# Kernel tuning notes

Measured on AMD Instinct MI355X. Metric: run time of the kernel, lower is better.

Reference implementation:

```python
import jax, jax.numpy as jnp
import numpy as np

B, C, HK, WK = 1, 128, 32, 32
S = 4                       # upsample factor hq/hk = dilation
HQ, WQ = HK * S, WK * S
NH = 4                      # heads
HD = C // NH                # head dim
KH = KW = 7                 # odd(max(3, round(2*0.1*32)))
DH = DW = S
EPS = float(jnp.finfo(jnp.float32).eps)  # torch RMSNorm default eps for fp32


def natten_indices(L, K, D):
    """NATTEN clamped-window key indices per query position. Returns [L, K] int array."""
    NS = K // 2
    i = np.arange(L)
    if D <= 1:
        start = np.maximum(i - NS, 0) + (i + NS >= L) * (L - i - NS - 1)
    else:
        ni = i - NS * D
        imodd = i % D
        a = (L // D) * D
        b = L - a
        far = np.where(imodd < b, L - b + imodd - 2 * NS * D, a + imodd - K * D)
        start = np.where(ni < 0, imodd, np.where(i + NS * D >= L, far, ni))
    return jnp.asarray(start[:, None] + np.arange(K)[None, :] * D)


def setup_inputs() -> dict:
    key = jax.random.key(0)
    ks = jax.random.split(key, 8)
    sc = 1.0 / np.sqrt(C)
    return {
        "q": jax.random.normal(ks[0], (B, C, HQ, WQ), jnp.float32),
        "k": jax.random.normal(ks[1], (B, C, HK, WK), jnp.float32),
        "v": jax.random.normal(ks[2], (B, C, HK, WK), jnp.float32),
        "conv_w": jax.random.normal(ks[3], (C, C, 3, 3), jnp.float32) * (sc / 3.0),
        "normq_w": 1.0 + 0.02 * jax.random.normal(ks[4], (C,), jnp.float32),
        "normk_w": 1.0 + 0.02 * jax.random.normal(ks[5], (C,), jnp.float32),
        "qproj_w": jax.random.normal(ks[6], (C, C), jnp.float32) * sc,
        "qproj_b": jnp.zeros((C,), jnp.float32),
        "kproj_w": jax.random.normal(ks[7], (C, C), jnp.float32) * sc,
        "kproj_b": jnp.zeros((C,), jnp.float32),
    }


def _rmsnorm(x, w):  # x: [B,C,H,W]; RMS over channel dim
    ms = jnp.mean(x * x, axis=1, keepdims=True)
    return x * jax.lax.rsqrt(ms + EPS) * w[None, :, None, None]


def reference(q, k, v, conv_w, normq_w, normk_w, qproj_w, qproj_b, kproj_w, kproj_b):
    # 3x3 conv on q (no bias, padding=1)
    q = jax.lax.conv_general_dilated(q, conv_w, (1, 1), "SAME",
                                     dimension_numbers=("NCHW", "OIHW", "NCHW"))
    q = _rmsnorm(q, normq_w)
    k = _rmsnorm(k, normk_w)
    # 1x1 projections (Conv2d k=1 with bias)
    q = jnp.einsum("oc,bchw->bohw", qproj_w, q) + qproj_b[None, :, None, None]
    k = jnp.einsum("oc,bchw->bohw", kproj_w, k) + kproj_b[None, :, None, None]
    # nearest-exact upsample of k, v to (HQ, WQ); integer factor -> exact pixel repeat
    k = jnp.repeat(jnp.repeat(k, S, axis=2), S, axis=3)
    v = jnp.repeat(jnp.repeat(v, S, axis=2), S, axis=3)
    # NATTEN layout [B, H, W, heads, hd]
    qn = q.reshape(B, NH, HD, HQ, WQ).transpose(0, 3, 4, 1, 2)
    kn = k.reshape(B, NH, HD, HQ, WQ).transpose(0, 3, 4, 1, 2)
    vh = v.transpose(0, 2, 3, 1)  # [B,HQ,WQ,C]; V is shared (expanded) across heads.
    # channel-pad-to-8 in the original is a no-op here since C % 8 == 0.
    ih = natten_indices(HQ, KH, DH)  # [HQ, KH]
    iw = natten_indices(WQ, KW, DW)  # [WQ, KW]
    k_nb = jnp.take(jnp.take(kn, ih, axis=1), iw, axis=3)  # [B,HQ,KH,WQ,KW,NH,HD]
    v_nb = jnp.take(jnp.take(vh, ih, axis=1), iw, axis=3)  # [B,HQ,KH,WQ,KW,C]
    scale = HD ** -0.5
    logits = jnp.einsum("bijhd,bimjnhd->bijhmn", qn, k_nb) * scale
    attn = jax.nn.softmax(logits.reshape(B, HQ, WQ, NH, KH * KW), axis=-1)
    attn = attn.reshape(B, HQ, WQ, NH, KH, KW)
    # heads share V, and the block takes mean over heads at the end; the mean
    # commutes with the (linear) V-contraction, so average attention first.
    attn_mean = attn.mean(axis=3)  # [B,HQ,WQ,KH,KW]
    out = jnp.einsum("bijmn,bimjnc->bcij", attn_mean, v_nb)  # [B,C,HQ,WQ]
    return out
```

## Files before the change

### kernel.cpp

```cpp
#include <hip/hip_runtime.h>

#define EPS_ 1.1920928955078125e-07f
#define SCALE_ 0.17677669529663687f

typedef __attribute__((ext_vector_type(8))) short s8b;
typedef __attribute__((ext_vector_type(4))) float f32x4;

static __device__ __forceinline__ unsigned short f2bf(float f) {
  unsigned int u = __float_as_uint(f);
  unsigned int r = (u + 0x7fffu + ((u >> 16) & 1u)) >> 16;
  return (unsigned short)r;
}
static __device__ __forceinline__ int S_(int c) {
  return (c < 3) ? 0 : ((c > 28) ? 25 : (c - 3));
}

__global__ __launch_bounds__(256) void wpack_k(
    const float* __restrict__ cw, const float* __restrict__ qw,
    const float* __restrict__ nqw, const float* __restrict__ kw,
    const float* __restrict__ nkw, unsigned short* __restrict__ wb,
    unsigned short* __restrict__ wnq, unsigned short* __restrict__ wnk) {
  int idx = blockIdx.x * 256 + threadIdx.x;
  if (idx < 147456) {
    int i32 = idx & 31, r = idx >> 5;
    int oc = r & 127, r2 = r >> 7;
    int kc = r2 & 3, t = r2 >> 2;
    wb[idx] = f2bf(cw[oc * 1152 + (kc * 32 + i32) * 9 + t]);
  } else if (idx < 163840) {
    int j = idx - 147456;
    wnq[j] = f2bf(qw[j] * nqw[j & 127]);
  } else if (idx < 180224) {
    int j = idx - 163840;
    wnk[j] = f2bf(kw[j] * nkw[j & 127]);
  }
}

__global__ __launch_bounds__(512) void fused_k(
    const float* __restrict__ q_in, const float* __restrict__ k_in,
    const float* __restrict__ v_in, const unsigned short* __restrict__ wb,
    const unsigned short* __restrict__ wnq, const unsigned short* __restrict__ wnk,
    const float* __restrict__ qbias, const float* __restrict__ kbias,
    float* __restrict__ out) {
  __shared__ __align__(16) char smem[65344];
  unsigned short* in_l = (unsigned short*)smem;
  unsigned short* qc_l = (unsigned short*)smem;
  unsigned short* a_l  = (unsigned short*)smem;
  float* o_l   = (float*)smem;
  unsigned short* kx_l = (unsigned short*)(smem + 27200);
  unsigned short* v_l  = (unsigned short*)(smem + 44608);
  float* red_l = (float*)(smem + 63040);
  float* rs_l  = (float*)(smem + 65088);

  const int tid = threadIdx.x;
  const int CY = blockIdx.x >> 4, CX = blockIdx.x & 15;
  const int Y0 = CY * 8, X0 = CX * 8;
  const int w = tid >> 6, lane = tid & 63;
  const int lm = lane & 15, kg = lane >> 4;
  const int mg = w & 1, ng = w >> 1;
  const int h = w >> 1, mh = w & 1;

  const int sy0 = S_(2 * CY), sy1 = S_(2 * CY + 1);
  const int sx0 = S_(2 * CX), sx1 = S_(2 * CX + 1);
  const int kyb = min(sy0, 24), kxb = min(sx0, 24);
  const int oy0 = sy0 - kyb, oy1 = sy1 - kyb;
  const int ox0 = sx0 - kxb, ox1 = sx1 - kxb;

  for (int i = tid; i < 12800; i += 512) {
    int c = i / 100, r = i - c * 100;
    int ry = r / 10, rx = r - ry * 10;
    int gy = Y0 - 1 + ry, gx = X0 - 1 + rx;
    float v = 0.f;
    if ((unsigned)gy < 128u && (unsigned)gx < 128u) v = q_in[c * 16384 + gy * 128 + gx];
    in_l[r * 136 + c] = f2bf(v);
  }
  {
    const int j = tid & 63, cg = tid >> 3 >> 3;
    const int ky = j >> 3, kx = j & 7;
    const float* kp = &k_in[(kyb + ky) * 32 + kxb + kx];
    float s = 0.f;
#pragma unroll
    for (int it = 0; it < 16; it++) {
      int c = cg * 16 + it;
      float v = kp[c * 1024];
      s += v * v;
      kx_l[j * 136 + c] = f2bf(v);
    }
    red_l[j * 8 + cg] = s;
  }
  {
    const int j = tid & 63, cg = tid >> 6;
    const int ky = j >> 3, kx = j & 7;
    const float* vp = &v_in[(kyb + ky) * 32 + kxb + kx];
#pragma unroll
    for (int it = 0; it < 16; it++) {
      int c = cg * 16 + it;
      v_l[c * 72 + j] = f2bf(vp[c * 1024]);
    }
  }
  __syncthreads();

  if (tid < 64) {
    float s = 0.f;
#pragma unroll
    for (int e = 0; e < 8; e++) s += red_l[tid * 8 + e];
    rs_l[tid] = rsqrtf(s * (1.f / 128.f) + EPS_);
  }
  __syncthreads();

  {
    f32x4 ka[4];
#pragma unroll
    for (int a = 0; a < 4; a++) ka[a] = (f32x4){0.f, 0.f, 0.f, 0.f};
#pragma unroll
    for (int kc = 0; kc < 4; kc++) {
      s8b af[4];
#pragma unroll
      for (int mt = 0; mt < 4; mt++)
        af[mt] = *(const s8b*)&wnk[((mg * 4 + mt) * 16 + lm) * 128 + kc * 32 + kg * 8];
      s8b bf = *(const s8b*)&kx_l[(ng * 16 + lm) * 136 + kc * 32 + kg * 8];
#pragma unroll
      for (int mt = 0; mt < 4; mt++)
        ka[mt] = __builtin_amdgcn_mfma_f32_16x16x32_bf16(af[mt], bf, ka[mt], 0, 0, 0);
    }
    __syncthreads();
    const int px = ng * 16 + lm;
    const float rs = rs_l[px];
#pragma unroll
    for (int mt = 0; mt < 4; mt++)
#pragma unroll
      for (int r = 0; r < 4; r++) {
        int c = (mg * 4 + mt) * 16 + kg * 4 + r;
        kx_l[px * 136 + c] = f2bf(kbias[c] + rs * ka[mt][r]);
      }
  }

  f32x4 acc[4];
#pragma unroll
  for (int a = 0; a < 4; a++) acc[a] = (f32x4){0.f, 0.f, 0.f, 0.f};
  const int pxc = ng * 16 + lm;
  const int qy = pxc >> 3, qx = pxc & 7;
#pragma unroll
  for (int t = 0; t < 9; t++) {
    const int dy = t / 3, dx = t - (t / 3) * 3;
#pragma unroll
    for (int kc = 0; kc < 4; kc++) {
      const unsigned short* wp = wb + (t * 4 + kc) * 4096;
      s8b af[4];
#pragma unroll
      for (int mt = 0; mt < 4; mt++)
        af[mt] = *(const s8b*)&wp[((mg * 4 + mt) * 16 + lm) * 32 + kg * 8];
      s8b bf = *(const s8b*)&in_l[((qy + dy) * 10 + qx + dx) * 136 + kc * 32 + kg * 8];
#pragma unroll
      for (int mt = 0; mt < 4; mt++)
        acc[mt] = __builtin_amdgcn_mfma_f32_16x16x32_bf16(af[mt], bf, acc[mt], 0, 0, 0);
    }
  }
  __syncthreads();
#pragma unroll
  for (int mt = 0; mt < 4; mt++)
#pragma unroll
    for (int r = 0; r < 4; r++) {
      int c = (mg * 4 + mt) * 16 + kg * 4 + r;
      qc_l[pxc * 136 + c] = f2bf(acc[mt][r]);
    }
  __syncthreads();

  {
    int px = tid >> 3, t8 = tid & 7;
    const unsigned short* row = &qc_l[px * 136 + t8 * 16];
    s8b v0 = *(const s8b*)row;
    s8b v1 = *(const s8b*)(row + 8);
    float s = 0.f;
#pragma unroll
    for (int e = 0; e < 8; e++) {
      float f0 = __uint_as_float(((unsigned)(unsigned short)v0[e]) << 16);
      float f1 = __uint_as_float(((unsigned)(unsigned short)v1[e]) << 16);
      s += f0 * f0 + f1 * f1;
    }
    red_l[px * 8 + t8] = s;
  }
  __syncthreads();
  if (tid < 64) {
    float s = 0.f;
#pragma unroll
    for (int e = 0; e < 8; e++) s += red_l[tid * 8 + e];
    rs_l[tid] = rsqrtf(s * (1.f / 128.f) + EPS_);
  }
  __syncthreads();

  {
    f32x4 qa[4];
#pragma unroll
    for (int a = 0; a < 4; a++) qa[a] = (f32x4){0.f, 0.f, 0.f, 0.f};
#pragma unroll
    for (int kc = 0; kc < 4; kc++) {
      s8b af[4];
#pragma unroll
      for (int mt = 0; mt < 4; mt++)
        af[mt] = *(const s8b*)&wnq[((mg * 4 + mt) * 16 + lm) * 128 + kc * 32 + kg * 8];
      s8b bf = *(const s8b*)&qc_l[(ng * 16 + lm) * 136 + kc * 32 + kg * 8];
#pragma unroll
      for (int mt = 0; mt < 4; mt++)
        qa[mt] = __builtin_amdgcn_mfma_f32_16x16x32_bf16(af[mt], bf, qa[mt], 0, 0, 0);
    }
    __syncthreads();
    const int px = ng * 16 + lm;
    const float rs = rs_l[px];
#pragma unroll
    for (int mt = 0; mt < 4; mt++)
#pragma unroll
      for (int r = 0; r < 4; r++) {
        int c = (mg * 4 + mt) * 16 + kg * 4 + r;
        qc_l[px * 136 + c] = f2bf(qbias[c] + rs * qa[mt][r]);
      }
  }
  __syncthreads();

  f32x4 lg[2][4];
  {
    s8b qa[2], kb[4];
#pragma unroll
    for (int mt = 0; mt < 2; mt++)
      qa[mt] = *(const s8b*)&qc_l[((mh * 2 + mt) * 16 + lm) * 136 + h * 32 + kg * 8];
#pragma unroll
    for (int nt = 0; nt < 4; nt++)
      kb[nt] = *(const s8b*)&kx_l[(nt * 16 + lm) * 136 + h * 32 + kg * 8];
#pragma unroll
    for (int mt = 0; mt < 2; mt++)
#pragma unroll
      for (int nt = 0; nt < 4; nt++)
        lg[mt][nt] = __builtin_amdgcn_mfma_f32_16x16x32_bf16(
            qa[mt], kb[nt], (f32x4){0.f, 0.f, 0.f, 0.f}, 0, 0, 0);
  }
  __syncthreads();

  {
    const int kyA = lm >> 3, kxq = lm & 7;
    const bool kxv0 = (unsigned)(kxq - ox0) < 7u;
    const bool kxv1 = (unsigned)(kxq - ox1) < 7u;
#pragma unroll
    for (int mt = 0; mt < 2; mt++) {
#pragma unroll
      for (int r = 0; r < 4; r++) {
        int j = (mh * 2 + mt) * 16 + kg * 4 + r;
        int oy = ((j >> 5) & 1) ? oy1 : oy0;
        bool kxv = ((j >> 2) & 1) ? kxv1 : kxv0;
        float l[4];
#pragma unroll
        for (int nt = 0; nt < 4; nt++) {
          int ky = 2 * nt + kyA;
          bool valid = kxv && ((unsigned)(ky - oy) < 7u);
          l[nt] = valid ? lg[mt][nt][r] * SCALE_ : -1e30f;
        }
        float mx = fmaxf(fmaxf(l[0], l[1]), fmaxf(l[2], l[3]));
#pragma unroll
        for (int off = 1; off < 16; off <<= 1) mx = fmaxf(mx, __shfl_xor(mx, off, 64));
        float e0 = __expf(l[0] - mx), e1 = __expf(l[1] - mx);
        float e2 = __expf(l[2] - mx), e3 = __expf(l[3] - mx);
        float ss = e0 + e1 + e2 + e3;
#pragma unroll
        for (int off = 1; off < 16; off <<= 1) ss += __shfl_xor(ss, off, 64);
        float inv = 1.f / ss;
        unsigned short* ap = &a_l[(h * 64 + j) * 72];
        ap[lm]      = f2bf(e0 * inv);
        ap[16 + lm] = f2bf(e1 * inv);
        ap[32 + lm] = f2bf(e2 * inv);
        ap[48 + lm] = f2bf(e3 * inv);
      }
    }
  }
  __syncthreads();

  f32x4 oacc[4];
#pragma unroll
  for (int a = 0; a < 4; a++) oacc[a] = (f32x4){0.f, 0.f, 0.f, 0.f};
#pragma unroll
  for (int kc = 0; kc < 2; kc++) {
    s8b vb2 = *(const s8b*)&v_l[(w * 16 + lm) * 72 + kc * 32 + kg * 8];
#pragma unroll
    for (int hh = 0; hh < 4; hh++) {
#pragma unroll
      for (int mt = 0; mt < 4; mt++) {
        s8b pa = *(const s8b*)&a_l[(hh * 64 + mt * 16 + lm) * 72 + kc * 32 + kg * 8];
        oacc[mt] = __builtin_amdgcn_mfma_f32_16x16x32_bf16(pa, vb2, oacc[mt], 0, 0, 0);
      }
    }
  }
  __syncthreads();

#pragma unroll
  for (int mt = 0; mt < 4; mt++)
#pragma unroll
    for (int r = 0; r < 4; r++)
      o_l[(w * 16 + lm) * 68 + mt * 16 + kg * 4 + r] = 0.25f * oacc[mt][r];
  __syncthreads();
  for (int i = tid; i < 2048; i += 512) {
    int c = i >> 4, rr = i & 15;
    int qyo = rr >> 1, hx = rr & 1;
    float4 v = *(const float4*)&o_l[c * 68 + qyo * 8 + hx * 4];
    *(float4*)&out[c * 16384 + (Y0 + qyo) * 128 + X0 + hx * 4] = v;
  }
}

extern "C" void kernel_launch(void* const* d_in, const int* in_sizes, int n_in,
                              void* d_out, int out_size, void* d_ws, size_t ws_size,
                              hipStream_t stream) {
  const float* q_in    = (const float*)d_in[0];
  const float* k_in    = (const float*)d_in[1];
  const float* v_in    = (const float*)d_in[2];
  const float* conv_w  = (const float*)d_in[3];
  const float* normq_w = (const float*)d_in[4];
  const float* normk_w = (const float*)d_in[5];
  const float* qproj_w = (const float*)d_in[6];
  const float* qproj_b = (const float*)d_in[7];
  const float* kproj_w = (const float*)d_in[8];
  const float* kproj_b = (const float*)d_in[9];
  float* out = (float*)d_out;

  char* ws = (char*)d_ws;
  unsigned short* wb  = (unsigned short*)(ws);
  unsigned short* wnq = (unsigned short*)(ws + 294912);
  unsigned short* wnk = (unsigned short*)(ws + 327680);

  wpack_k<<<dim3(704), 256, 0, stream>>>(conv_w, qproj_w, normq_w, kproj_w, normk_w,
                                         wb, wnq, wnk);
  fused_k<<<dim3(256), 512, 0, stream>>>(q_in, k_in, v_in, wb, wnq, wnk,
                                         qproj_b, kproj_b, out);
}
```

Baseline: 120.7 us.

## Precompute padded bf16 channel-last Q and projected K in prep kernel

A new prep kernel converts q into a zero-padded bf16 NHWC buffer and computes the normalized and projected K once per key pixel, storing it as bf16. The main fused kernel then loads halo tiles with 16-byte vector copies instead of strided fp32 gathers, and it no longer repeats the K RMSNorm and projection GEMM in every block. The cost is an extra global round trip of about 4 MB of bf16 q and a larger workspace. Work is also moved out of the main kernel into the prep launch.

```diff
diff --git a/kernel.cpp b/kernel.cpp
--- a/kernel.cpp
+++ b/kernel.cpp
@@ -11,35 +11,139 @@
   unsigned int r = (u + 0x7fffu + ((u >> 16) & 1u)) >> 16;
   return (unsigned short)r;
 }
+static __device__ __forceinline__ float b2fs(short h) {
+  return __uint_as_float(((unsigned int)(unsigned short)h) << 16);
+}
 static __device__ __forceinline__ int S_(int c) {
   return (c < 3) ? 0 : ((c > 28) ? 25 : (c - 3));
 }
 
-__global__ __launch_bounds__(256) void wpack_k(
-    const float* __restrict__ cw, const float* __restrict__ qw,
-    const float* __restrict__ nqw, const float* __restrict__ kw,
-    const float* __restrict__ nkw, unsigned short* __restrict__ wb,
-    unsigned short* __restrict__ wnq, unsigned short* __restrict__ wnk) {
-  int idx = blockIdx.x * 256 + threadIdx.x;
-  if (idx < 147456) {
-    int i32 = idx & 31, r = idx >> 5;
-    int oc = r & 127, r2 = r >> 7;
-    int kc = r2 & 3, t = r2 >> 2;
-    wb[idx] = f2bf(cw[oc * 1152 + (kc * 32 + i32) * 9 + t]);
-  } else if (idx < 163840) {
-    int j = idx - 147456;
-    wnq[j] = f2bf(qw[j] * nqw[j & 127]);
-  } else if (idx < 180224) {
-    int j = idx - 163840;
-    wnk[j] = f2bf(kw[j] * nkw[j & 127]);
+__global__ __launch_bounds__(256) void prep_k(
+    const float* __restrict__ q_in, const float* __restrict__ k_in,
+    const float* __restrict__ conv_w, const float* __restrict__ normq_w,
+    const float* __restrict__ normk_w, const float* __restrict__ qproj_w,
+    const float* __restrict__ kproj_w, const float* __restrict__ kbias,
+    unsigned short* __restrict__ qb, unsigned short* __restrict__ kpb,
+    unsigned short* __restrict__ wb, unsigned short* __restrict__ wnq) {
+  __shared__ __align__(16) char smem[53504];
+  unsigned short* t_l = (unsigned short*)smem;
+  unsigned short* x_l = (unsigned short*)smem;
+  unsigned short* wnk_l = (unsigned short*)(smem + 17408);
+  float* red_l = (float*)(smem + 52224);
+  float* rs_l  = (float*)(smem + 53248);
+  const int b = blockIdx.x, tid = threadIdx.x;
+  const int w = tid >> 6, lane = tid & 63;
+  const int lm = lane & 15, kg = lane >> 4;
+
+  if (b < 256) {
+    const int px0 = b * 64;
+    for (int i = tid; i < 2048; i += 256) {
+      int c = i >> 4, f = i & 15;
+      float4 v = *(const float4*)&q_in[c * 16384 + px0 + f * 4];
+      t_l[(f * 4 + 0) * 136 + c] = f2bf(v.x);
+      t_l[(f * 4 + 1) * 136 + c] = f2bf(v.y);
+      t_l[(f * 4 + 2) * 136 + c] = f2bf(v.z);
+      t_l[(f * 4 + 3) * 136 + c] = f2bf(v.w);
+    }
+    __syncthreads();
+    for (int i = tid; i < 1024; i += 256) {
+      int p = i >> 4, s = i & 15;
+      int px = px0 + p;
+      int opx = px + 2 * (px >> 7) + 131;
+      *(s8b*)&qb[opx * 128 + s * 8] = *(const s8b*)&t_l[p * 136 + s * 8];
+    }
+  } else if (b < 265) {
+    int gid = (b - 256) * 256 + tid;
+    s8b z = {0, 0, 0, 0, 0, 0, 0, 0};
+    for (int j = gid; j < 2080; j += 2304) {
+      *(s8b*)&qb[j * 8] = z;
+      *(s8b*)&qb[129 * 130 * 128 + j * 8] = z;
+    }
+    for (int j = gid; j < 2048; j += 2304) {
+      int r = (j >> 4) + 1, s = j & 15;
+      *(s8b*)&qb[(r * 130) * 128 + s * 8] = z;
+      *(s8b*)&qb[(r * 130 + 129) * 128 + s * 8] = z;
+    }
+  } else if (b < 281) {
+    const int px0 = (b - 265) * 64;
+    for (int i = tid; i < 2048; i += 256) {
+      int c = i >> 4, f = i & 15;
+      float4 v = *(const float4*)&k_in[c * 1024 + px0 + f * 4];
+      x_l[(f * 4 + 0) * 136 + c] = f2bf(v.x);
+      x_l[(f * 4 + 1) * 136 + c] = f2bf(v.y);
+      x_l[(f * 4 + 2) * 136 + c] = f2bf(v.z);
+      x_l[(f * 4 + 3) * 136 + c] = f2bf(v.w);
+    }
+    for (int i = tid; i < 16384; i += 256) {
+      int o = i >> 7, c = i & 127;
+      wnk_l[o * 136 + c] = f2bf(kproj_w[i] * normk_w[c]);
+    }
+    __syncthreads();
+    {
+      int px = tid >> 2, t4 = tid & 3;
+      float ssum = 0.f;
+#pragma unroll
+      for (int j = 0; j < 4; j++) {
+        s8b v = *(const s8b*)&x_l[px * 136 + t4 * 32 + j * 8];
+#pragma unroll
+        for (int e = 0; e < 8; e++) { float f = b2fs(v[e]); ssum += f * f; }
+      }
+      red_l[px * 4 + t4] = ssum;
+    }
+    __syncthreads();
+    if (tid < 64)
+      rs_l[tid] = rsqrtf((red_l[4 * tid] + red_l[4 * tid + 1] + red_l[4 * tid + 2] +
+                          red_l[4 * tid + 3]) * (1.f / 128.f) + EPS_);
+    __syncthreads();
+    f32x4 acc[2][4];
+#pragma unroll
+    for (int a = 0; a < 2; a++)
+#pragma unroll
+      for (int n = 0; n < 4; n++) acc[a][n] = (f32x4){0.f, 0.f, 0.f, 0.f};
+#pragma unroll
+    for (int kc = 0; kc < 4; kc++) {
+      s8b a0 = *(const s8b*)&wnk_l[(2 * w * 16 + lm) * 136 + kc * 32 + kg * 8];
+      s8b a1 = *(const s8b*)&wnk_l[((2 * w + 1) * 16 + lm) * 136 + kc * 32 + kg * 8];
+#pragma unroll
+      for (int nt = 0; nt < 4; nt++) {
+        s8b bf = *(const s8b*)&x_l[(nt * 16 + lm) * 136 + kc * 32 + kg * 8];
+        acc[0][nt] = __builtin_amdgcn_mfma_f32_16x16x32_bf16(a0, bf, acc[0][nt], 0, 0, 0);
+        acc[1][nt] = __builtin_amdgcn_mfma_f32_16x16x32_bf16(a1, bf, acc[1][nt], 0, 0, 0);
+      }
+    }
+    __syncthreads();
+#pragma unroll
+    for (int mi = 0; mi < 2; mi++)
+#pragma unroll
+      for (int nt = 0; nt < 4; nt++)
+#pragma unroll
+        for (int r = 0; r < 4; r++) {
+          int px = nt * 16 + lm, c = (2 * w + mi) * 16 + kg * 4 + r;
+          x_l[px * 136 + c] = f2bf(kbias[c] + rs_l[px] * acc[mi][nt][r]);
+        }
+    __syncthreads();
+    for (int i = tid; i < 1024; i += 256) {
+      int px = i >> 4, s = i & 15;
+      *(s8b*)&kpb[(px0 + px) * 128 + s * 8] = *(const s8b*)&x_l[px * 136 + s * 8];
+    }
+  } else {
+    int idx = (b - 281) * 256 + tid;
+    if (idx < 147456) {
+      int i32 = idx & 31, r = idx >> 5;
+      int oc = r & 127, r2 = r >> 7;
+      int kc = r2 & 3, t = r2 >> 2;
+      wb[idx] = f2bf(conv_w[oc * 1152 + (kc * 32 + i32) * 9 + t]);
+    } else {
+      int j = idx - 147456;
+      wnq[j] = f2bf(qproj_w[j] * normq_w[j & 127]);
+    }
   }
 }
 
 __global__ __launch_bounds__(512) void fused_k(
-    const float* __restrict__ q_in, const float* __restrict__ k_in,
+    const unsigned short* __restrict__ qb, const unsigned short* __restrict__ kpb,
     const float* __restrict__ v_in, const unsigned short* __restrict__ wb,
-    const unsigned short* __restrict__ wnq, const unsigned short* __restrict__ wnk,
-    const float* __restrict__ qbias, const float* __restrict__ kbias,
+    const unsigned short* __restrict__ wnq, const float* __restrict__ qbias,
     float* __restrict__ out) {
   __shared__ __align__(16) char smem[65344];
   unsigned short* in_l = (unsigned short*)smem;
@@ -65,27 +169,17 @@
   const int oy0 = sy0 - kyb, oy1 = sy1 - kyb;
   const int ox0 = sx0 - kxb, ox1 = sx1 - kxb;
 
-  for (int i = tid; i < 12800; i += 512) {
-    int c = i / 100, r = i - c * 100;
+  for (int i = tid; i < 1600; i += 512) {
+    int s = i & 15, r = i >> 4;
     int ry = r / 10, rx = r - ry * 10;
-    int gy = Y0 - 1 + ry, gx = X0 - 1 + rx;
-    float v = 0.f;
-    if ((unsigned)gy < 128u && (unsigned)gx < 128u) v = q_in[c * 16384 + gy * 128 + gx];
-    in_l[r * 136 + c] = f2bf(v);
-  }
-  {
-    const int j = tid & 63, cg = tid >> 3 >> 3;
-    const int ky = j >> 3, kx = j & 7;
-    const float* kp = &k_in[(kyb + ky) * 32 + kxb + kx];
-    float s = 0.f;
-#pragma unroll
-    for (int it = 0; it < 16; it++) {
-      int c = cg * 16 + it;
-      float v = kp[c * 1024];
-      s += v * v;
-      kx_l[j * 136 + c] = f2bf(v);
-    }
-    red_l[j * 8 + cg] = s;
+    *(s8b*)&in_l[r * 136 + s * 8] =
+        *(const s8b*)&qb[((Y0 + ry) * 130 + X0 + rx) * 128 + s * 8];
+  }
+  for (int i = tid; i < 1024; i += 512) {
+    int j = i >> 4, s = i & 15;
+    int ky = j >> 3, kx = j & 7;
+    *(s8b*)&kx_l[j * 136 + s * 8] =
+        *(const s8b*)&kpb[((kyb + ky) * 32 + kxb + kx) * 128 + s * 8];
   }
   {
     const int j = tid & 63, cg = tid >> 6;
@@ -98,41 +192,6 @@
     }
   }
   __syncthreads();
-
-  if (tid < 64) {
-    float s = 0.f;
-#pragma unroll
-    for (int e = 0; e < 8; e++) s += red_l[tid * 8 + e];
-    rs_l[tid] = rsqrtf(s * (1.f / 128.f) + EPS_);
-  }
-  __syncthreads();
-
-  {
-    f32x4 ka[4];
-#pragma unroll
-    for (int a = 0; a < 4; a++) ka[a] = (f32x4){0.f, 0.f, 0.f, 0.f};
-#pragma unroll
-    for (int kc = 0; kc < 4; kc++) {
-      s8b af[4];
-#pragma unroll
-      for (int mt = 0; mt < 4; mt++)
-        af[mt] = *(const s8b*)&wnk[((mg * 4 + mt) * 16 + lm) * 128 + kc * 32 + kg * 8];
-      s8b bf = *(const s8b*)&kx_l[(ng * 16 + lm) * 136 + kc * 32 + kg * 8];
-#pragma unroll
-      for (int mt = 0; mt < 4; mt++)
-        ka[mt] = __builtin_amdgcn_mfma_f32_16x16x32_bf16(af[mt], bf, ka[mt], 0, 0, 0);
-    }
-    __syncthreads();
-    const int px = ng * 16 + lm;
-    const float rs = rs_l[px];
-#pragma unroll
-    for (int mt = 0; mt < 4; mt++)
-#pragma unroll
-      for (int r = 0; r < 4; r++) {
-        int c = (mg * 4 + mt) * 16 + kg * 4 + r;
-        kx_l[px * 136 + c] = f2bf(kbias[c] + rs * ka[mt][r]);
-      }
-  }
 
   f32x4 acc[4];
 #pragma unroll
@@ -173,8 +232,7 @@
     float s = 0.f;
 #pragma unroll
     for (int e = 0; e < 8; e++) {
-      float f0 = __uint_as_float(((unsigned)(unsigned short)v0[e]) << 16);
-      float f1 = __uint_as_float(((unsigned)(unsigned short)v1[e]) << 16);
+      float f0 = b2fs(v0[e]), f1 = b2fs(v1[e]);
       s += f0 * f0 + f1 * f1;
     }
     red_l[px * 8 + t8] = s;
@@ -198,20 +256,19 @@
 #pragma unroll
       for (int mt = 0; mt < 4; mt++)
         af[mt] = *(const s8b*)&wnq[((mg * 4 + mt) * 16 + lm) * 128 + kc * 32 + kg * 8];
-      s8b bf = *(const s8b*)&qc_l[(ng * 16 + lm) * 136 + kc * 32 + kg * 8];
+      s8b bf = *(const s8b*)&qc_l[pxc * 136 + kc * 32 + kg * 8];
 #pragma unroll
       for (int mt = 0; mt < 4; mt++)
         qa[mt] = __builtin_amdgcn_mfma_f32_16x16x32_bf16(af[mt], bf, qa[mt], 0, 0, 0);
     }
     __syncthreads();
-    const int px = ng * 16 + lm;
-    const float rs = rs_l[px];
+    const float rs = rs_l[pxc];
 #pragma unroll
     for (int mt = 0; mt < 4; mt++)
 #pragma unroll
       for (int r = 0; r < 4; r++) {
         int c = (mg * 4 + mt) * 16 + kg * 4 + r;
-        qc_l[px * 136 + c] = f2bf(qbias[c] + rs * qa[mt][r]);
+        qc_l[pxc * 136 + c] = f2bf(qbias[c] + rs * qa[mt][r]);
       }
   }
   __syncthreads();
@@ -318,12 +375,13 @@
   float* out = (float*)d_out;
 
   char* ws = (char*)d_ws;
-  unsigned short* wb  = (unsigned short*)(ws);
-  unsigned short* wnq = (unsigned short*)(ws + 294912);
-  unsigned short* wnk = (unsigned short*)(ws + 327680);
-
-  wpack_k<<<dim3(704), 256, 0, stream>>>(conv_w, qproj_w, normq_w, kproj_w, normk_w,
-                                         wb, wnq, wnk);
-  fused_k<<<dim3(256), 512, 0, stream>>>(q_in, k_in, v_in, wb, wnq, wnk,
-                                         qproj_b, kproj_b, out);
-}
+  unsigned short* qb  = (unsigned short*)(ws);
+  unsigned short* kpb = (unsigned short*)(ws + 4326400);
+  unsigned short* wb  = (unsigned short*)(ws + 4588544);
+  unsigned short* wnq = (unsigned short*)(ws + 4883456);
+
+  prep_k<<<dim3(921), 256, 0, stream>>>(q_in, k_in, conv_w, normq_w, normk_w,
+                                        qproj_w, kproj_w, kproj_b,
+                                        qb, kpb, wb, wnq);
+  fused_k<<<dim3(256), 512, 0, stream>>>(qb, kpb, v_in, wb, wnq, qproj_b, out);
+}
```

Result: no change. 118.9 us (-1.5%).
